# Kernel tuning notes

Measured on AMD Instinct MI355X. Metric: run time of the kernel, lower is better.

Reference implementation:

```python
import jax, jax.numpy as jnp
import numpy as np

DIM = 1024
HID = 2732  # int(2*4*1024/3) rounded up to multiple of 4
E = 8
TOPK = 2
B, S = 2, 2048


def setup_inputs() -> dict:
    key = jax.random.key(0)
    ks = jax.random.split(key, 5)
    scale = 0.02
    return {
        "x": jax.random.normal(ks[0], (B, S, DIM), dtype=jnp.float32),
        "Wg": jax.random.normal(ks[1], (E, DIM), dtype=jnp.float32) * scale,
        "W1": jax.random.normal(ks[2], (E, HID, DIM), dtype=jnp.float32) * scale,
        "W2": jax.random.normal(ks[3], (E, DIM, HID), dtype=jnp.float32) * scale,
        "W3": jax.random.normal(ks[4], (E, HID, DIM), dtype=jnp.float32) * scale,
    }


def reference(x, Wg, W1, W2, W3):
    b, s, d = x.shape
    xt = x.reshape(b * s, d)                              # [N, d]
    scores = xt @ Wg.T                                    # [N, E]
    w, idx = jax.lax.top_k(scores, TOPK)                  # [N, k]
    w = jax.nn.softmax(w, axis=-1)
    n = xt.shape[0]
    # combine weights scattered back into [N, E] (top-k indices are distinct per row)
    cw = jnp.zeros((n, E), dtype=x.dtype).at[jnp.arange(n)[:, None], idx].set(w)
    # dense per-expert SwiGLU (mathematically identical to masked dispatch)
    h1 = jnp.einsum('nd,ehd->neh', xt, W1)                # [N, E, H]
    h3 = jnp.einsum('nd,ehd->neh', xt, W3)
    h = jax.nn.silu(h1) * h3
    y = jnp.einsum('neh,edh->ned', h, W2)                 # [N, E, d]
    out = jnp.einsum('ned,ne->nd', y, cw)                 # [N, d]
    return out
```

## Files before the change

### kernel.cpp

```cpp
#include <hip/hip_runtime.h>
#include <hip/hip_bf16.h>
#include <stdint.h>

#define DIM   1024
#define HID   2732
#define HPAD  2816
#define NEXP  8
#define NTOK  4096
#define NROW  8192

typedef __attribute__((ext_vector_type(8))) short bf16x8;
typedef __attribute__((ext_vector_type(4))) float f32x4;

__device__ __forceinline__ unsigned short f2bf(float f) {
    union { float f; uint32_t u; } v; v.f = f;
    uint32_t u = v.u;
    return (unsigned short)((u + 0x7FFFu + ((u >> 16) & 1u)) >> 16);
}

#define ASYNC_CP16(g, l) __builtin_amdgcn_global_load_lds( \
    (const __attribute__((address_space(1))) void*)(g), \
    (__attribute__((address_space(3))) void*)(l), 16, 0, 0)

__global__ void conv_w13_kernel(const float* __restrict__ src,
                                unsigned short* __restrict__ dst) {
    size_t t = (size_t)blockIdx.x * 256 + threadIdx.x;
    int d4 = (int)(t & 255);
    size_t rest = t >> 8;
    int hp = (int)(rest % HPAD);
    int e  = (int)(rest / HPAD);
    ushort4 o;
    if (hp < HID) {
        float4 v = *(const float4*)(src + ((size_t)e * HID + hp) * DIM + d4 * 4);
        o.x = f2bf(v.x); o.y = f2bf(v.y); o.z = f2bf(v.z); o.w = f2bf(v.w);
    } else {
        o.x = o.y = o.z = o.w = 0;
    }
    *(ushort4*)(dst + t * 4) = o;
}

__global__ void conv_w2_kernel(const float* __restrict__ src,
                               unsigned short* __restrict__ dst) {
    size_t t = (size_t)blockIdx.x * 256 + threadIdx.x;
    int h4 = (int)(t % (HPAD / 4));
    size_t rest = t / (HPAD / 4);
    int d = (int)(rest % DIM);
    int e = (int)(rest / DIM);
    ushort4 o;
    if (h4 * 4 < HID) {
        float4 v = *(const float4*)(src + ((size_t)e * DIM + d) * HID + h4 * 4);
        o.x = f2bf(v.x); o.y = f2bf(v.y); o.z = f2bf(v.z); o.w = f2bf(v.w);
    } else {
        o.x = o.y = o.z = o.w = 0;
    }
    *(ushort4*)(dst + t * 4) = o;
}

__global__ void route_kernel(const float* __restrict__ x, const float* __restrict__ Wg,
                             int* __restrict__ counts, int* __restrict__ a_exp,
                             int* __restrict__ a_rank, float* __restrict__ a_w) {
    int wave = threadIdx.x >> 6, lane = threadIdx.x & 63;
    int n = blockIdx.x * 4 + wave;
    const float* xr = x + (size_t)n * DIM + lane * 16;
    float p[NEXP];
#pragma unroll
    for (int e = 0; e < NEXP; ++e) p[e] = 0.f;
#pragma unroll
    for (int i = 0; i < 4; ++i) {
        float4 xv = *(const float4*)(xr + i * 4);
#pragma unroll
        for (int e = 0; e < NEXP; ++e) {
            float4 wv = *(const float4*)(Wg + e * DIM + lane * 16 + i * 4);
            p[e] += xv.x * wv.x + xv.y * wv.y + xv.z * wv.z + xv.w * wv.w;
        }
    }
#pragma unroll
    for (int off = 32; off > 0; off >>= 1)
#pragma unroll
        for (int e = 0; e < NEXP; ++e) p[e] += __shfl_xor(p[e], off);
    if (lane == 0) {
        int i1 = -1, i2 = -1; float m1 = -1e30f, m2 = -1e30f;
#pragma unroll
        for (int e = 0; e < NEXP; ++e) {
            float s = p[e];
            if (s > m1) { m2 = m1; i2 = i1; m1 = s; i1 = e; }
            else if (s > m2) { m2 = s; i2 = e; }
        }
        float e2 = __expf(m2 - m1);
        float inv = 1.f / (1.f + e2);
        int a = n * 2;
        a_exp[a] = i1;  a_w[a] = inv;        a_rank[a] = atomicAdd(&counts[i1], 1);
        a_exp[a+1] = i2; a_w[a+1] = e2 * inv; a_rank[a+1] = atomicAdd(&counts[i2], 1);
    }
}

__global__ void scan_kernel(const int* __restrict__ counts, int* __restrict__ offsets) {
    if (threadIdx.x == 0) {
        int s = 0;
        for (int e = 0; e < NEXP; ++e) { offsets[e] = s; s += counts[e]; }
    }
}

__global__ void gather_kernel(const float* __restrict__ x, const int* __restrict__ a_exp,
                              const int* __restrict__ a_rank,
                              const int* __restrict__ offsets,
                              unsigned short* __restrict__ XG,
                              int* __restrict__ row_of_a) {
    int a = blockIdx.x, n = a >> 1;
    int row = offsets[a_exp[a]] + a_rank[a];
    if (threadIdx.x == 0) row_of_a[a] = row;
    float4 xv = *(const float4*)(x + (size_t)n * DIM + threadIdx.x * 4);
    ushort4 o; o.x = f2bf(xv.x); o.y = f2bf(xv.y); o.z = f2bf(xv.z); o.w = f2bf(xv.w);
    *(ushort4*)(XG + (size_t)row * DIM + threadIdx.x * 4) = o;
}

__global__ __launch_bounds__(256, 2) void gemm1_kernel(
    const unsigned short* __restrict__ XG,
    const unsigned short* __restrict__ W1b,
    const unsigned short* __restrict__ W3b,
    const int* __restrict__ counts, const int* __restrict__ offsets,
    unsigned short* __restrict__ Hbuf)
{
    const int e = blockIdx.z, mtile = blockIdx.y, ntile = blockIdx.x;
    const int cnt = counts[e];
    if (mtile * 128 >= cnt) return;
    const int rowstart = offsets[e] + mtile * 128;

    __shared__ __align__(16) unsigned short As[128 * 64];
    __shared__ __align__(16) unsigned short B1s[64 * 64];
    __shared__ __align__(16) unsigned short B3s[64 * 64];

    const int tid = threadIdx.x, lane = tid & 63, wave = tid >> 6;
    const int wm = wave >> 1, wn = wave & 1;
    const int quad = lane >> 4;

    const unsigned short* w1e = W1b + (size_t)e * HPAD * DIM;
    const unsigned short* w3e = W3b + (size_t)e * HPAD * DIM;

    const int srow = tid >> 3;
    const int scol = (((tid & 7) ^ (srow & 7)) * 8);
    const unsigned short* ag[4];
#pragma unroll
    for (int r = 0; r < 4; ++r) {
        int grow = rowstart + r * 32 + srow;
        if (grow > NROW - 1) grow = NROW - 1;
        ag[r] = XG + (size_t)grow * DIM + scol;
    }
    const unsigned short* bg1[2]; const unsigned short* bg3[2];
#pragma unroll
    for (int r = 0; r < 2; ++r) {
        int grow = ntile * 64 + r * 32 + srow;
        bg1[r] = w1e + (size_t)grow * DIM + scol;
        bg3[r] = w3e + (size_t)grow * DIM + scol;
    }

    f32x4 acc1[4][2], acc3[4][2];
#pragma unroll
    for (int i = 0; i < 4; ++i)
#pragma unroll
        for (int j = 0; j < 2; ++j) {
            acc1[i][j] = (f32x4){0.f, 0.f, 0.f, 0.f};
            acc3[i][j] = (f32x4){0.f, 0.f, 0.f, 0.f};
        }

    for (int kk = 0; kk < DIM / 64; ++kk) {
        const int k0 = kk * 64;
#pragma unroll
        for (int r = 0; r < 4; ++r)
            ASYNC_CP16(ag[r] + k0, &As[r * 2048 + tid * 8]);
#pragma unroll
        for (int r = 0; r < 2; ++r) {
            ASYNC_CP16(bg1[r] + k0, &B1s[r * 2048 + tid * 8]);
            ASYNC_CP16(bg3[r] + k0, &B3s[r * 2048 + tid * 8]);
        }
        __syncthreads();
#pragma unroll
        for (int ks = 0; ks < 2; ++ks) {
            const int cbase = ks * 4 + quad;
            bf16x8 af[4], b1f[2], b3f[2];
#pragma unroll
            for (int i = 0; i < 4; ++i) {
                int rl = wm * 64 + i * 16 + (lane & 15);
                af[i] = *(const bf16x8*)&As[rl * 64 + ((cbase ^ (rl & 7)) * 8)];
            }
#pragma unroll
            for (int j = 0; j < 2; ++j) {
                int rl1 = wn * 32 + j * 16 + (lane & 15);
                b1f[j] = *(const bf16x8*)&B1s[rl1 * 64 + ((cbase ^ (rl1 & 7)) * 8)];
                b3f[j] = *(const bf16x8*)&B3s[rl1 * 64 + ((cbase ^ (rl1 & 7)) * 8)];
            }
#pragma unroll
            for (int i = 0; i < 4; ++i)
#pragma unroll
                for (int j = 0; j < 2; ++j) {
                    acc1[i][j] = __builtin_amdgcn_mfma_f32_16x16x32_bf16(af[i], b1f[j], acc1[i][j], 0, 0, 0);
                    acc3[i][j] = __builtin_amdgcn_mfma_f32_16x16x32_bf16(af[i], b3f[j], acc3[i][j], 0, 0, 0);
                }
        }
        __syncthreads();
    }

    int mvalid = cnt - mtile * 128; if (mvalid > 128) mvalid = 128;
#pragma unroll
    for (int i = 0; i < 4; ++i)
#pragma unroll
        for (int r = 0; r < 4; ++r) {
            int rl = wm * 64 + i * 16 + quad * 4 + r;
            if (rl < mvalid) {
                size_t rowg = (size_t)(rowstart + rl);
#pragma unroll
                for (int j = 0; j < 2; ++j) {
                    float v1 = acc1[i][j][r], v3 = acc3[i][j][r];
                    float s = v1 / (1.f + __expf(-v1));
                    Hbuf[rowg * HPAD + ntile * 64 + wn * 32 + j * 16 + (lane & 15)] = f2bf(s * v3);
                }
            }
        }
}

__global__ __launch_bounds__(256, 2) void gemm2_kernel(
    const unsigned short* __restrict__ Hbuf,
    const unsigned short* __restrict__ W2b,
    const int* __restrict__ counts, const int* __restrict__ offsets,
    float* __restrict__ Ybuf)
{
    const int e = blockIdx.z, mtile = blockIdx.y, ntile = blockIdx.x;
    const int cnt = counts[e];
    if (mtile * 128 >= cnt) return;
    const int rowstart = offsets[e] + mtile * 128;

    __shared__ __align__(16) unsigned short As[128 * 64];
    __shared__ __align__(16) unsigned short Bs[128 * 64];

    const int tid = threadIdx.x, lane = tid & 63, wave = tid >> 6;
    const int wm = wave >> 1, wn = wave & 1;
    const int quad = lane >> 4;

    const unsigned short* w2e = W2b + (size_t)e * DIM * HPAD;
    const int srow = tid >> 3;
    const int scol = (((tid & 7) ^ (srow & 7)) * 8);
    const unsigned short* ag[4]; const unsigned short* bg[4];
#pragma unroll
    for (int r = 0; r < 4; ++r) {
        int grow = rowstart + r * 32 + srow;
        if (grow > NROW - 1) grow = NROW - 1;
        ag[r] = Hbuf + (size_t)grow * HPAD + scol;
        bg[r] = w2e + (size_t)(ntile * 128 + r * 32 + srow) * HPAD + scol;
    }

    f32x4 acc[4][4];
#pragma unroll
    for (int i = 0; i < 4; ++i)
#pragma unroll
        for (int j = 0; j < 4; ++j) acc[i][j] = (f32x4){0.f, 0.f, 0.f, 0.f};

    for (int kk = 0; kk < HPAD / 64; ++kk) {
        const int k0 = kk * 64;
#pragma unroll
        for (int r = 0; r < 4; ++r) {
            ASYNC_CP16(ag[r] + k0, &As[r * 2048 + tid * 8]);
            ASYNC_CP16(bg[r] + k0, &Bs[r * 2048 + tid * 8]);
        }
        __syncthreads();
#pragma unroll
        for (int ks = 0; ks < 2; ++ks) {
            const int cbase = ks * 4 + quad;
            bf16x8 af[4], bf[4];
#pragma unroll
            for (int i = 0; i < 4; ++i) {
                int rla = wm * 64 + i * 16 + (lane & 15);
                int rlb = wn * 64 + i * 16 + (lane & 15);
                af[i] = *(const bf16x8*)&As[rla * 64 + ((cbase ^ (rla & 7)) * 8)];
                bf[i] = *(const bf16x8*)&Bs[rlb * 64 + ((cbase ^ (rlb & 7)) * 8)];
            }
#pragma unroll
            for (int i = 0; i < 4; ++i)
#pragma unroll
                for (int j = 0; j < 4; ++j)
                    acc[i][j] = __builtin_amdgcn_mfma_f32_16x16x32_bf16(af[i], bf[j], acc[i][j], 0, 0, 0);
        }
        __syncthreads();
    }

    int mvalid = cnt - mtile * 128; if (mvalid > 128) mvalid = 128;
#pragma unroll
    for (int i = 0; i < 4; ++i)
#pragma unroll
        for (int r = 0; r < 4; ++r) {
            int rl = wm * 64 + i * 16 + quad * 4 + r;
            if (rl < mvalid) {
                int rowg = rowstart + rl;
                float* yrow = Ybuf + (size_t)rowg * DIM + ntile * 128 + wn * 64 + (lane & 15);
#pragma unroll
                for (int j = 0; j < 4; ++j)
                    yrow[j * 16] = acc[i][j][r];
            }
        }
}

__global__ void combine_kernel(const float* __restrict__ Ybuf,
                               const int* __restrict__ row_of_a,
                               const float* __restrict__ a_w,
                               float* __restrict__ out) {
    int n = blockIdx.x, t = threadIdx.x;
    int r0 = row_of_a[2 * n], r1 = row_of_a[2 * n + 1];
    float w0 = a_w[2 * n], w1 = a_w[2 * n + 1];
    float4 y0 = *(const float4*)(Ybuf + (size_t)r0 * DIM + t * 4);
    float4 y1 = *(const float4*)(Ybuf + (size_t)r1 * DIM + t * 4);
    float4 o;
    o.x = w0 * y0.x + w1 * y1.x;
    o.y = w0 * y0.y + w1 * y1.y;
    o.z = w0 * y0.z + w1 * y1.z;
    o.w = w0 * y0.w + w1 * y1.w;
    *(float4*)(out + (size_t)n * DIM + t * 4) = o;
}

extern "C" void kernel_launch(void* const* d_in, const int* in_sizes, int n_in,
                              void* d_out, int out_size, void* d_ws, size_t ws_size,
                              hipStream_t stream) {
    const float* x  = (const float*)d_in[0];
    const float* Wg = (const float*)d_in[1];
    const float* W1 = (const float*)d_in[2];
    const float* W2 = (const float*)d_in[3];
    const float* W3 = (const float*)d_in[4];
    float* out = (float*)d_out;

    char* ws = (char*)d_ws;
    size_t off = 0;
    auto alloc = [&](size_t bytes) -> void* {
        void* p = ws + off;
        off = (off + bytes + 255) & ~(size_t)255;
        return p;
    };
    int*   counts      = (int*)alloc(NEXP * 4);
    int*   offsets     = (int*)alloc(NEXP * 4);
    int*   a_exp       = (int*)alloc(NROW * 4);
    int*   a_rank      = (int*)alloc(NROW * 4);
    float* a_w         = (float*)alloc(NROW * 4);
    int*   row_of_a    = (int*)alloc(NROW * 4);
    unsigned short* XG   = (unsigned short*)alloc((size_t)NROW * DIM * 2);
    unsigned short* Hbuf = (unsigned short*)alloc((size_t)NROW * HPAD * 2);
    unsigned short* W1b  = (unsigned short*)alloc((size_t)NEXP * HPAD * DIM * 2);
    unsigned short* W3b  = (unsigned short*)alloc((size_t)NEXP * HPAD * DIM * 2);
    unsigned short* W2b  = (unsigned short*)alloc((size_t)NEXP * DIM * HPAD * 2);
    float* Ybuf = (float*)W1b;

    hipMemsetAsync(counts, 0, NEXP * 4, stream);

    const int convBlocks = (NEXP * HPAD * DIM / 4) / 256;
    conv_w13_kernel<<<convBlocks, 256, 0, stream>>>(W1, W1b);
    conv_w13_kernel<<<convBlocks, 256, 0, stream>>>(W3, W3b);
    conv_w2_kernel<<<convBlocks, 256, 0, stream>>>(W2, W2b);

    route_kernel<<<NTOK / 4, 256, 0, stream>>>(x, Wg, counts, a_exp, a_rank, a_w);
    scan_kernel<<<1, 64, 0, stream>>>(counts, offsets);
    gather_kernel<<<NROW, 256, 0, stream>>>(x, a_exp, a_rank, offsets, XG, row_of_a);

    gemm1_kernel<<<dim3(HPAD / 64, 64, NEXP), 256, 0, stream>>>(
        XG, W1b, W3b, counts, offsets, Hbuf);
    gemm2_kernel<<<dim3(DIM / 128, 64, NEXP), 256, 0, stream>>>(
        Hbuf, W2b, counts, offsets, Ybuf);
    combine_kernel<<<NTOK, 256, 0, stream>>>(Ybuf, row_of_a, a_w, out);
}
```

Baseline: 597.4 us.

## Merge weight conversion and routing into one launch, drop scan kernel, store Y as bf16

Result: faster. 575.9 us (-3.6%).

```diff
diff --git a/kernel.cpp b/kernel.cpp
--- a/kernel.cpp
+++ b/kernel.cpp
@@ -8,6 +8,7 @@
 #define NEXP  8
 #define NTOK  4096
 #define NROW  8192
+#define C13BLK 22528
 
 typedef __attribute__((ext_vector_type(8))) short bf16x8;
 typedef __attribute__((ext_vector_type(4))) float f32x4;
@@ -17,14 +18,18 @@
     uint32_t u = v.u;
     return (unsigned short)((u + 0x7FFFu + ((u >> 16) & 1u)) >> 16);
 }
+__device__ __forceinline__ float bf2f(unsigned short h) {
+    union { uint32_t u; float f; } v; v.u = ((uint32_t)h) << 16;
+    return v.f;
+}
 
 #define ASYNC_CP16(g, l) __builtin_amdgcn_global_load_lds( \
     (const __attribute__((address_space(1))) void*)(g), \
     (__attribute__((address_space(3))) void*)(l), 16, 0, 0)
 
-__global__ void conv_w13_kernel(const float* __restrict__ src,
-                                unsigned short* __restrict__ dst) {
-    size_t t = (size_t)blockIdx.x * 256 + threadIdx.x;
+__device__ __forceinline__ void conv13_body(const float* __restrict__ src,
+                                            unsigned short* __restrict__ dst, int blk) {
+    size_t t = (size_t)blk * 256 + threadIdx.x;
     int d4 = (int)(t & 255);
     size_t rest = t >> 8;
     int hp = (int)(rest % HPAD);
@@ -39,28 +44,38 @@
     *(ushort4*)(dst + t * 4) = o;
 }
 
-__global__ void conv_w2_kernel(const float* __restrict__ src,
-                               unsigned short* __restrict__ dst) {
-    size_t t = (size_t)blockIdx.x * 256 + threadIdx.x;
-    int h4 = (int)(t % (HPAD / 4));
-    size_t rest = t / (HPAD / 4);
-    int d = (int)(rest % DIM);
-    int e = (int)(rest / DIM);
-    ushort4 o;
-    if (h4 * 4 < HID) {
-        float4 v = *(const float4*)(src + ((size_t)e * DIM + d) * HID + h4 * 4);
-        o.x = f2bf(v.x); o.y = f2bf(v.y); o.z = f2bf(v.z); o.w = f2bf(v.w);
-    } else {
-        o.x = o.y = o.z = o.w = 0;
-    }
-    *(ushort4*)(dst + t * 4) = o;
-}
-
-__global__ void route_kernel(const float* __restrict__ x, const float* __restrict__ Wg,
-                             int* __restrict__ counts, int* __restrict__ a_exp,
-                             int* __restrict__ a_rank, float* __restrict__ a_w) {
+__global__ void prep_kernel(const float* __restrict__ x,  const float* __restrict__ Wg,
+                            const float* __restrict__ W1, const float* __restrict__ W2,
+                            const float* __restrict__ W3,
+                            unsigned short* __restrict__ W1b,
+                            unsigned short* __restrict__ W2b,
+                            unsigned short* __restrict__ W3b,
+                            int* __restrict__ counts, int* __restrict__ a_exp,
+                            int* __restrict__ a_rank, float* __restrict__ a_w) {
+    int b = blockIdx.x;
+    if (b < C13BLK) { conv13_body(W1, W1b, b); return; }
+    b -= C13BLK;
+    if (b < C13BLK) { conv13_body(W3, W3b, b); return; }
+    b -= C13BLK;
+    if (b < C13BLK) {
+        size_t t = (size_t)b * 256 + threadIdx.x;
+        int h4 = (int)(t % (HPAD / 4));
+        size_t rest = t / (HPAD / 4);
+        int d = (int)(rest % DIM);
+        int e = (int)(rest / DIM);
+        ushort4 o;
+        if (h4 * 4 < HID) {
+            float4 v = *(const float4*)(W2 + ((size_t)e * DIM + d) * HID + h4 * 4);
+            o.x = f2bf(v.x); o.y = f2bf(v.y); o.z = f2bf(v.z); o.w = f2bf(v.w);
+        } else {
+            o.x = o.y = o.z = o.w = 0;
+        }
+        *(ushort4*)(W2b + t * 4) = o;
+        return;
+    }
+    b -= C13BLK;
     int wave = threadIdx.x >> 6, lane = threadIdx.x & 63;
-    int n = blockIdx.x * 4 + wave;
+    int n = b * 4 + wave;
     const float* xr = x + (size_t)n * DIM + lane * 16;
     float p[NEXP];
 #pragma unroll
@@ -94,20 +109,20 @@
     }
 }
 
-__global__ void scan_kernel(const int* __restrict__ counts, int* __restrict__ offsets) {
+__global__ void gather_kernel(const float* __restrict__ x, const int* __restrict__ a_exp,
+                              const int* __restrict__ a_rank,
+                              const int* __restrict__ counts,
+                              unsigned short* __restrict__ XG,
+                              int* __restrict__ row_of_a) {
+    __shared__ int soff[NEXP];
     if (threadIdx.x == 0) {
         int s = 0;
-        for (int e = 0; e < NEXP; ++e) { offsets[e] = s; s += counts[e]; }
-    }
-}
-
-__global__ void gather_kernel(const float* __restrict__ x, const int* __restrict__ a_exp,
-                              const int* __restrict__ a_rank,
-                              const int* __restrict__ offsets,
-                              unsigned short* __restrict__ XG,
-                              int* __restrict__ row_of_a) {
+#pragma unroll
+        for (int e = 0; e < NEXP; ++e) { soff[e] = s; s += counts[e]; }
+    }
+    __syncthreads();
     int a = blockIdx.x, n = a >> 1;
-    int row = offsets[a_exp[a]] + a_rank[a];
+    int row = soff[a_exp[a]] + a_rank[a];
     if (threadIdx.x == 0) row_of_a[a] = row;
     float4 xv = *(const float4*)(x + (size_t)n * DIM + threadIdx.x * 4);
     ushort4 o; o.x = f2bf(xv.x); o.y = f2bf(xv.y); o.z = f2bf(xv.z); o.w = f2bf(xv.w);
@@ -118,13 +133,15 @@
     const unsigned short* __restrict__ XG,
     const unsigned short* __restrict__ W1b,
     const unsigned short* __restrict__ W3b,
-    const int* __restrict__ counts, const int* __restrict__ offsets,
+    const int* __restrict__ counts,
     unsigned short* __restrict__ Hbuf)
 {
     const int e = blockIdx.z, mtile = blockIdx.y, ntile = blockIdx.x;
     const int cnt = counts[e];
     if (mtile * 128 >= cnt) return;
-    const int rowstart = offsets[e] + mtile * 128;
+    int rowstart = 0;
+    for (int i = 0; i < e; ++i) rowstart += counts[i];
+    rowstart += mtile * 128;
 
     __shared__ __align__(16) unsigned short As[128 * 64];
     __shared__ __align__(16) unsigned short B1s[64 * 64];
@@ -221,13 +238,15 @@
 __global__ __launch_bounds__(256, 2) void gemm2_kernel(
     const unsigned short* __restrict__ Hbuf,
     const unsigned short* __restrict__ W2b,
-    const int* __restrict__ counts, const int* __restrict__ offsets,
-    float* __restrict__ Ybuf)
+    const int* __restrict__ counts,
+    unsigned short* __restrict__ Ybuf)
 {
     const int e = blockIdx.z, mtile = blockIdx.y, ntile = blockIdx.x;
     const int cnt = counts[e];
     if (mtile * 128 >= cnt) return;
-    const int rowstart = offsets[e] + mtile * 128;
+    int rowstart = 0;
+    for (int i = 0; i < e; ++i) rowstart += counts[i];
+    rowstart += mtile * 128;
 
     __shared__ __align__(16) unsigned short As[128 * 64];
     __shared__ __align__(16) unsigned short Bs[128 * 64];
@@ -290,28 +309,28 @@
             int rl = wm * 64 + i * 16 + quad * 4 + r;
             if (rl < mvalid) {
                 int rowg = rowstart + rl;
-                float* yrow = Ybuf + (size_t)rowg * DIM + ntile * 128 + wn * 64 + (lane & 15);
+                unsigned short* yrow = Ybuf + (size_t)rowg * DIM + ntile * 128 + wn * 64 + (lane & 15);
 #pragma unroll
                 for (int j = 0; j < 4; ++j)
-                    yrow[j * 16] = acc[i][j][r];
-            }
-        }
-}
-
-__global__ void combine_kernel(const float* __restrict__ Ybuf,
+                    yrow[j * 16] = f2bf(acc[i][j][r]);
+            }
+        }
+}
+
+__global__ void combine_kernel(const unsigned short* __restrict__ Ybuf,
                                const int* __restrict__ row_of_a,
                                const float* __restrict__ a_w,
                                float* __restrict__ out) {
     int n = blockIdx.x, t = threadIdx.x;
     int r0 = row_of_a[2 * n], r1 = row_of_a[2 * n + 1];
     float w0 = a_w[2 * n], w1 = a_w[2 * n + 1];
-    float4 y0 = *(const float4*)(Ybuf + (size_t)r0 * DIM + t * 4);
-    float4 y1 = *(const float4*)(Ybuf + (size_t)r1 * DIM + t * 4);
+    ushort4 y0 = *(const ushort4*)(Ybuf + (size_t)r0 * DIM + t * 4);
+    ushort4 y1 = *(const ushort4*)(Ybuf + (size_t)r1 * DIM + t * 4);
     float4 o;
-    o.x = w0 * y0.x + w1 * y1.x;
-    o.y = w0 * y0.y + w1 * y1.y;
-    o.z = w0 * y0.z + w1 * y1.z;
-    o.w = w0 * y0.w + w1 * y1.w;
+    o.x = w0 * bf2f(y0.x) + w1 * bf2f(y1.x);
+    o.y = w0 * bf2f(y0.y) + w1 * bf2f(y1.y);
+    o.z = w0 * bf2f(y0.z) + w1 * bf2f(y1.z);
+    o.w = w0 * bf2f(y0.w) + w1 * bf2f(y1.w);
     *(float4*)(out + (size_t)n * DIM + t * 4) = o;
 }
 
@@ -333,7 +352,6 @@
         return p;
     };
     int*   counts      = (int*)alloc(NEXP * 4);
-    int*   offsets     = (int*)alloc(NEXP * 4);
     int*   a_exp       = (int*)alloc(NROW * 4);
     int*   a_rank      = (int*)alloc(NROW * 4);
     float* a_w         = (float*)alloc(NROW * 4);
@@ -343,22 +361,17 @@
     unsigned short* W1b  = (unsigned short*)alloc((size_t)NEXP * HPAD * DIM * 2);
     unsigned short* W3b  = (unsigned short*)alloc((size_t)NEXP * HPAD * DIM * 2);
     unsigned short* W2b  = (unsigned short*)alloc((size_t)NEXP * DIM * HPAD * 2);
-    float* Ybuf = (float*)W1b;
+    unsigned short* Ybuf = (unsigned short*)W1b;
 
     hipMemsetAsync(counts, 0, NEXP * 4, stream);
 
-    const int convBlocks = (NEXP * HPAD * DIM / 4) / 256;
-    conv_w13_kernel<<<convBlocks, 256, 0, stream>>>(W1, W1b);
-    conv_w13_kernel<<<convBlocks, 256, 0, stream>>>(W3, W3b);
-    conv_w2_kernel<<<convBlocks, 256, 0, stream>>>(W2, W2b);
-
-    route_kernel<<<NTOK / 4, 256, 0, stream>>>(x, Wg, counts, a_exp, a_rank, a_w);
-    scan_kernel<<<1, 64, 0, stream>>>(counts, offsets);
-    gather_kernel<<<NROW, 256, 0, stream>>>(x, a_exp, a_rank, offsets, XG, row_of_a);
+    prep_kernel<<<3 * C13BLK + NTOK / 4, 256, 0, stream>>>(
+        x, Wg, W1, W2, W3, W1b, W2b, W3b, counts, a_exp, a_rank, a_w);
+    gather_kernel<<<NROW, 256, 0, stream>>>(x, a_exp, a_rank, counts, XG, row_of_a);
 
     gemm1_kernel<<<dim3(HPAD / 64, 64, NEXP), 256, 0, stream>>>(
-        XG, W1b, W3b, counts, offsets, Hbuf);
+        XG, W1b, W3b, counts, Hbuf);
     gemm2_kernel<<<dim3(DIM / 128, 64, NEXP), 256, 0, stream>>>(
-        Hbuf, W2b, counts, offsets, Ybuf);
+        Hbuf, W2b, counts, Ybuf);
     combine_kernel<<<NTOK, 256, 0, stream>>>(Ybuf, row_of_a, a_w, out);
 }
```
